# Kernel optimization log

Hardware: AMD Instinct MI355X
Metric: run time of the kernel (lower is better)

The kernel has to match this reference:

```python
import jax, jax.numpy as jnp
import numpy as np

D_MODEL = 1024
D_STATE = 16
B, L = 4, 2048


def _ln(x, g, b, eps=1e-5):
    mu = x.mean(-1, keepdims=True)
    var = ((x - mu) ** 2).mean(-1, keepdims=True)
    return (x - mu) * jax.lax.rsqrt(var + eps) * g + b


def _selective_ssm(x, dt_w, dt_b, Bp_w, Bp_b, Cp_w, Cp_b, A_log, D_p):
    # x: (B, L, D)
    delta = jax.nn.softplus(x @ dt_w + dt_b)          # (B, L, D)
    Bt = x @ Bp_w + Bp_b                               # (B, L, N)
    Ct = x @ Cp_w + Cp_b                               # (B, L, N)
    A = -jnp.exp(A_log)                                # (D, N)

    def step(h, inp):
        xt, dt, bt, ct = inp                            # (B,D),(B,D),(B,N),(B,N)
        dA = jnp.exp(dt[..., None] * A)                 # (B, D, N)
        dBx = dt[..., None] * bt[:, None, :] * xt[..., None]
        h = dA * h + dBx                                # (B, D, N)
        y = jnp.einsum('bdn,bn->bd', h, ct)
        return h, y

    xs = (jnp.swapaxes(x, 0, 1), jnp.swapaxes(delta, 0, 1),
          jnp.swapaxes(Bt, 0, 1), jnp.swapaxes(Ct, 0, 1))
    h0 = jnp.zeros((x.shape[0], D_MODEL, D_STATE), dtype=x.dtype)
    _, ys = jax.lax.scan(step, h0, xs)                  # (L, B, D)
    return jnp.swapaxes(ys, 0, 1) + D_p * x


def _forward(x, ln1_g, ln1_b, ln_g, ln_b, w1_w, w1_b, v1_w, v1_b, w2_w, w2_b,
             conv_w, dt_w, dt_b, Bp_w, Bp_b, Cp_w, Cp_b, A_log, D_p,
             ln2_g, ln2_b, ff1_w, ff1_b, ff2_w, ff2_b):
    res = x
    xn = _ln(x, ln1_g, ln1_b)
    # --- MambaLayer ---
    xm = _ln(xn, ln_g, ln_b)
    x1 = xm @ w1_w + w1_b                               # (B, L, D)
    x1t = jnp.swapaxes(x1, 1, 2)                        # (B, D, L)
    xc = jax.lax.conv_general_dilated(
        x1t, conv_w, window_strides=(1,), padding=[(1, 1)],
        feature_group_count=D_MODEL,
        dimension_numbers=('NCH', 'OIH', 'NCH'))
    xc = jax.nn.silu(jnp.swapaxes(xc, 1, 2))            # (B, L, D)
    y = _selective_ssm(xc, dt_w, dt_b, Bp_w, Bp_b, Cp_w, Cp_b, A_log, D_p)
    v = jax.nn.silu(xm @ v1_w + v1_b)
    mo = (y * v) @ w2_w + w2_b
    # --- residual + FFN ---
    x = mo + res
    res2 = x
    xn2 = _ln(x, ln2_g, ln2_b)
    h = jax.nn.gelu(xn2 @ ff1_w + ff1_b, approximate=False)
    return h @ ff2_w + ff2_b + res2


def setup_inputs() -> dict:
    key = jax.random.key(0)
    ks = jax.random.split(key, 16)
    s = 0.02
    d, n = D_MODEL, D_STATE
    inp = {
        'x': jax.random.normal(ks[0], (B, L, d), jnp.float32),
        'ln1_g': jnp.ones((d,), jnp.float32), 'ln1_b': jnp.zeros((d,), jnp.float32),
        'ln_g': jnp.ones((d,), jnp.float32), 'ln_b': jnp.zeros((d,), jnp.float32),
        'w1_w': jax.random.normal(ks[1], (d, d), jnp.float32) * s,
        'w1_b': jnp.zeros((d,), jnp.float32),
        'v1_w': jax.random.normal(ks[2], (d, d), jnp.float32) * s,
        'v1_b': jnp.zeros((d,), jnp.float32),
        'w2_w': jax.random.normal(ks[3], (d, d), jnp.float32) * s,
        'w2_b': jnp.zeros((d,), jnp.float32),
        'conv_w': jax.random.normal(ks[4], (d, 1, 3), jnp.float32) * s,
        'dt_w': jax.random.normal(ks[5], (d, d), jnp.float32) * s,
        'dt_b': jnp.zeros((d,), jnp.float32),
        'Bp_w': jax.random.normal(ks[6], (d, n), jnp.float32) * s,
        'Bp_b': jnp.zeros((n,), jnp.float32),
        'Cp_w': jax.random.normal(ks[7], (d, n), jnp.float32) * s,
        'Cp_b': jnp.zeros((n,), jnp.float32),
        'A_log': jnp.tile(jnp.log(jnp.arange(1, n + 1, dtype=jnp.float32)), (d, 1)),
        'D_p': jnp.ones((d,), jnp.float32),
        'ln2_g': jnp.ones((d,), jnp.float32), 'ln2_b': jnp.zeros((d,), jnp.float32),
        'ff1_w': jax.random.normal(ks[8], (d, 3 * d), jnp.float32) * s,
        'ff1_b': jnp.zeros((3 * d,), jnp.float32),
        'ff2_w': jax.random.normal(ks[9], (3 * d, d), jnp.float32) * s,
        'ff2_b': jnp.zeros((d,), jnp.float32),
    }
    return inp


def reference(x, ln1_g, ln1_b, ln_g, ln_b, w1_w, w1_b, v1_w, v1_b, w2_w, w2_b,
              conv_w, dt_w, dt_b, Bp_w, Bp_b, Cp_w, Cp_b, A_log, D_p,
              ln2_g, ln2_b, ff1_w, ff1_b, ff2_w, ff2_b):
    return _forward(x, ln1_g, ln1_b, ln_g, ln_b, w1_w, w1_b, v1_w, v1_b, w2_w,
                    w2_b, conv_w, dt_w, dt_b, Bp_w, Bp_b, Cp_w, Cp_b, A_log,
                    D_p, ln2_g, ln2_b, ff1_w, ff1_b, ff2_w, ff2_b)
```

## Files before the change

kernel.cpp:

```cpp
#include <hip/hip_runtime.h>

typedef unsigned short u16;
typedef __attribute__((ext_vector_type(8))) short short8;
typedef __attribute__((ext_vector_type(4))) float f32x4;
typedef __attribute__((ext_vector_type(4))) unsigned short u16x4;

#define SEQ 2048
#define DM 1024
#define NTOK 8192
#define CH 64
#define NCH 32

__device__ __forceinline__ float b2f(u16 u) {
  union { float f; unsigned int i; } x; x.i = ((unsigned int)u) << 16; return x.f;
}
__device__ __forceinline__ u16 f2b(float f) {
  union { float f; unsigned int i; } x; x.f = f;
  unsigned int i = x.i;
  unsigned int r = (i + 0x7FFFu + ((i >> 16) & 1u)) >> 16;
  return (u16)r;
}

__device__ __forceinline__ void gload16(const u16* g, u16* l) {
  __builtin_amdgcn_global_load_lds(
      (const __attribute__((address_space(1))) void*)g,
      (__attribute__((address_space(3))) void*)l, 16, 0, 0);
}

__global__ __launch_bounds__(256)
void wtrans(const float* __restrict__ in, u16* __restrict__ out,
            int K, int N, int rowOff, int ldOut)
{
  __shared__ float tile[32][33];
  const int n0 = blockIdx.x * 32;
  const int k0 = blockIdx.y * 32;
  const int tx = threadIdx.x, ty = threadIdx.y;
#pragma unroll
  for (int i = 0; i < 32; i += 8) {
    int k = k0 + ty + i, n = n0 + tx;
    tile[ty + i][tx] = (k < K && n < N) ? in[(long)k * N + n] : 0.f;
  }
  __syncthreads();
#pragma unroll
  for (int i = 0; i < 32; i += 8) {
    int n = n0 + ty + i, k = k0 + tx;
    if (n < N && k < K) out[(long)(rowOff + n) * ldOut + k] = f2b(tile[tx][ty + i]);
  }
}

__global__ __launch_bounds__(256)
void small_trans(const float* __restrict__ Bp, const float* __restrict__ Cp,
                 u16* __restrict__ wcatT)
{
  int t = blockIdx.x * 256 + threadIdx.x;
  int n = t >> 10, k = t & 1023;
  wcatT[(long)(1024 + n) * 1024 + k] = f2b(Bp[(long)k * 16 + n]);
  wcatT[(long)(1040 + n) * 1024 + k] = f2b(Cp[(long)k * 16 + n]);
}

__device__ __forceinline__ void blockReduce2(float& a, float& b, float* s)
{
#pragma unroll
  for (int off = 32; off > 0; off >>= 1) {
    a += __shfl_xor(a, off);
    b += __shfl_xor(b, off);
  }
  const int lane = threadIdx.x & 63, wid = threadIdx.x >> 6;
  __syncthreads();
  if (lane == 0) { s[wid] = a; s[4 + wid] = b; }
  __syncthreads();
  a = s[0] + s[1] + s[2] + s[3];
  b = s[4] + s[5] + s[6] + s[7];
}

__global__ __launch_bounds__(256)
void ln_ln_kernel(const float* __restrict__ x, const float* __restrict__ g1,
                  const float* __restrict__ b1, const float* __restrict__ g2,
                  const float* __restrict__ b2, u16* __restrict__ out)
{
  __shared__ float sred[8];
  const long row = blockIdx.x;
  const int t = threadIdx.x;
  const float4 xv = ((const float4*)(x + row * DM))[t];
  float s = xv.x + xv.y + xv.z + xv.w;
  float sq = xv.x * xv.x + xv.y * xv.y + xv.z * xv.z + xv.w * xv.w;
  blockReduce2(s, sq, sred);
  const float mu = s * (1.f / DM);
  const float rs = rsqrtf(sq * (1.f / DM) - mu * mu + 1e-5f);
  const float4 g1v = ((const float4*)g1)[t];
  const float4 b1v = ((const float4*)b1)[t];
  float xn[4];
  xn[0] = (xv.x - mu) * rs * g1v.x + b1v.x;
  xn[1] = (xv.y - mu) * rs * g1v.y + b1v.y;
  xn[2] = (xv.z - mu) * rs * g1v.z + b1v.z;
  xn[3] = (xv.w - mu) * rs * g1v.w + b1v.w;
  float s2 = xn[0] + xn[1] + xn[2] + xn[3];
  float sq2 = xn[0] * xn[0] + xn[1] * xn[1] + xn[2] * xn[2] + xn[3] * xn[3];
  blockReduce2(s2, sq2, sred);
  const float mu2 = s2 * (1.f / DM);
  const float rs2 = rsqrtf(sq2 * (1.f / DM) - mu2 * mu2 + 1e-5f);
  const float4 g2v = ((const float4*)g2)[t];
  const float4 b2v = ((const float4*)b2)[t];
  u16x4 o;
  o[0] = f2b((xn[0] - mu2) * rs2 * g2v.x + b2v.x);
  o[1] = f2b((xn[1] - mu2) * rs2 * g2v.y + b2v.y);
  o[2] = f2b((xn[2] - mu2) * rs2 * g2v.z + b2v.z);
  o[3] = f2b((xn[3] - mu2) * rs2 * g2v.w + b2v.w);
  *(u16x4*)(out + row * DM + t * 4) = o;
}

__global__ __launch_bounds__(256)
void ln_kernel(const float* __restrict__ x, const float* __restrict__ g,
               const float* __restrict__ b, u16* __restrict__ out)
{
  __shared__ float sred[8];
  const long row = blockIdx.x;
  const int t = threadIdx.x;
  const float4 xv = ((const float4*)(x + row * DM))[t];
  float s = xv.x + xv.y + xv.z + xv.w;
  float sq = xv.x * xv.x + xv.y * xv.y + xv.z * xv.z + xv.w * xv.w;
  blockReduce2(s, sq, sred);
  const float mu = s * (1.f / DM);
  const float rs = rsqrtf(sq * (1.f / DM) - mu * mu + 1e-5f);
  const float4 gv = ((const float4*)g)[t];
  const float4 bv = ((const float4*)b)[t];
  u16x4 o;
  o[0] = f2b((xv.x - mu) * rs * gv.x + bv.x);
  o[1] = f2b((xv.y - mu) * rs * gv.y + bv.y);
  o[2] = f2b((xv.z - mu) * rs * gv.z + bv.z);
  o[3] = f2b((xv.w - mu) * rs * gv.w + bv.w);
  *(u16x4*)(out + row * DM + t * 4) = o;
}

__global__ __launch_bounds__(256)
void conv_silu_kernel(const u16* __restrict__ x1, const float* __restrict__ w,
                      u16* __restrict__ xc)
{
  const long i8 = (long)blockIdx.x * 256 + threadIdx.x;
  const long base = i8 * 8;
  const int d0 = (int)(base & (DM - 1));
  const long m = base >> 10;
  const int l = (int)(m & (SEQ - 1));
  const short8 cv = *(const short8*)(x1 + base);
  short8 lv = {}, rv = {};
  if (l > 0) lv = *(const short8*)(x1 + base - DM);
  if (l < SEQ - 1) rv = *(const short8*)(x1 + base + DM);
  short8 o;
#pragma unroll
  for (int j = 0; j < 8; ++j) {
    const int d = d0 + j;
    const float a = b2f((u16)lv[j]) * w[d * 3 + 0] + b2f((u16)cv[j]) * w[d * 3 + 1]
                  + b2f((u16)rv[j]) * w[d * 3 + 2];
    o[j] = (short)f2b(a / (1.f + __expf(-a)));
  }
  *(short8*)(xc + base) = o;
}

template <int MODE>
__global__ __launch_bounds__(256)
void gemm_bt(const u16* __restrict__ A, const u16* __restrict__ BT,
             const float* __restrict__ bias, const float* __restrict__ bias2,
             const float* __restrict__ bias3, const float* __restrict__ resid,
             void* __restrict__ outp, void* __restrict__ outp2,
             int K, int ldOut, int nbx)
{
  __shared__ u16 lds_a[2][4096];
  __shared__ u16 lds_b[2][4096];
  const int t = threadIdx.x;
  const int lane = t & 63;
  const int wid = t >> 6;
  const int wr = wid >> 1, wc = wid & 1;

  int bid = blockIdx.x;
  const int qch = gridDim.x >> 3;
  bid = (bid & 7) * qch + (bid >> 3);
  const long brow = (long)(bid / nbx) * 128;
  const long bcol = (long)(bid % nbx) * 128;

  f32x4 acc[4][4] = {};

  const int srow = t >> 2;
  const int sslot = (t & 3) ^ ((t >> 3) & 3);
  const u16* aPtr = A + (brow + srow) * (long)K + sslot * 8;
  const u16* bPtr = BT + (bcol + srow) * (long)K + sslot * 8;
  u16* la = &lds_a[0][t * 8];
  u16* lb = &lds_b[0][t * 8];
  const long rowStep = 64L * K;
  const int nk = K >> 5;

  const int rslot = (lane >> 4) ^ ((lane >> 1) & 3);
  const int koff = rslot * 8;
  const int arow = wr * 64 + (lane & 15);
  const int brw = wc * 64 + (lane & 15);

#define STAGE(kt, buf)                                              \
  {                                                                 \
    const int k0_ = (kt) << 5;                                      \
    gload16(aPtr + k0_, la + (buf) * 4096);                         \
    gload16(aPtr + rowStep + k0_, la + (buf) * 4096 + 2048);        \
    gload16(bPtr + k0_, lb + (buf) * 4096);                         \
    gload16(bPtr + rowStep + k0_, lb + (buf) * 4096 + 2048);        \
  }

  STAGE(0, 0);
  __syncthreads();
  int cur = 0;
  for (int kt = 0; kt < nk; ++kt) {
    if (kt + 1 < nk) STAGE(kt + 1, cur ^ 1);
    short8 af[4], bfr[4];
#pragma unroll
    for (int m = 0; m < 4; ++m)
      af[m] = *(const short8*)&lds_a[cur][(arow + m * 16) * 32 + koff];
#pragma unroll
    for (int n = 0; n < 4; ++n)
      bfr[n] = *(const short8*)&lds_b[cur][(brw + n * 16) * 32 + koff];
#pragma unroll
    for (int m = 0; m < 4; ++m)
#pragma unroll
      for (int n = 0; n < 4; ++n)
        acc[m][n] = __builtin_amdgcn_mfma_f32_16x16x32_bf16(af[m], bfr[n], acc[m][n], 0, 0, 0);
    __syncthreads();
    cur ^= 1;
  }
#undef STAGE

  const int cc = lane & 15;
  const int r0 = (lane >> 4) * 4;
#pragma unroll
  for (int m = 0; m < 4; ++m) {
#pragma unroll
    for (int n = 0; n < 4; ++n) {
      const long col = bcol + wc * 64 + n * 16 + cc;
#pragma unroll
      for (int r = 0; r < 4; ++r) {
        const long row = brow + wr * 64 + m * 16 + r0 + r;
        float val = acc[m][n][r];
        if constexpr (MODE == 4) {
          if (col < 1024) {
            val += bias[col];
            val = (val > 20.f) ? val : log1pf(__expf(val));
            ((float*)outp)[row * 1152 + col] = val;
          } else if (col < 1040) {
            ((float*)outp)[row * 1152 + col] = val + bias2[col - 1024];
          } else if (col < 1056) {
            ((float*)outp)[row * 1152 + col] = val + bias3[col - 1040];
          }
        } else if constexpr (MODE == 5) {
          if (col < 1024) {
            val += bias[col];
            ((u16*)outp)[row * 1024 + col] = f2b(val);
          } else {
            val += bias2[col - 1024];
            val = val / (1.f + __expf(-val));
            ((u16*)outp2)[row * 1024 + col - 1024] = f2b(val);
          }
        } else {
          val += bias[col];
          if constexpr (MODE == 2) val = 0.5f * val * (1.f + erff(val * 0.70710678118f));
          if constexpr (MODE == 3) {
            ((float*)outp)[row * ldOut + col] = val + resid[row * ldOut + col];
          } else {
            ((u16*)outp)[row * ldOut + col] = f2b(val);
          }
        }
      }
    }
  }
}

__global__ __launch_bounds__(256)
void scan_pass1(const u16* __restrict__ xc, const float* __restrict__ dtbc,
                const float* __restrict__ A_log, float* __restrict__ hloc,
                float* __restrict__ sdt)
{
  const int bx = blockIdx.x;
  const int b = bx >> 9;
  const int ch = (bx >> 4) & 31;
  const int dBase = (bx & 15) * 64;
  const int t = threadIdx.x;
  const int dl = t >> 2;
  const int q = t & 3;
  const int d = dBase + dl;

  __shared__ float s_b[32][16];
  __shared__ float s_dt[32][64];
  __shared__ u16 s_x[32][64];

  float Areg[4];
#pragma unroll
  for (int j = 0; j < 4; ++j) Areg[j] = -__expf(A_log[d * 16 + q * 4 + j]);
  float h[4] = {0.f, 0.f, 0.f, 0.f};
  float sAcc = 0.f;
  const long mBase = (long)b * SEQ + ch * CH;

  for (int c0 = 0; c0 < CH; c0 += 32) {
#pragma unroll
    for (int i = 0; i < 2; ++i) {
      int idx = i * 256 + t;
      int s = idx >> 4, j = idx & 15;
      s_b[s][j] = dtbc[(mBase + c0 + s) * 1152 + 1024 + j];
    }
#pragma unroll
    for (int i = 0; i < 8; ++i) {
      int idx = i * 256 + t;
      int s = idx >> 6, j = idx & 63;
      long m = mBase + c0 + s;
      s_dt[s][j] = dtbc[m * 1152 + dBase + j];
      s_x[s][j] = xc[m * DM + dBase + j];
    }
    __syncthreads();
#pragma unroll 4
    for (int s = 0; s < 32; ++s) {
      const float dt = s_dt[s][dl];
      const float p = dt * b2f(s_x[s][dl]);
      sAcc += dt;
#pragma unroll
      for (int j = 0; j < 4; ++j)
        h[j] = __expf(dt * Areg[j]) * h[j] + p * s_b[s][q * 4 + j];
    }
    __syncthreads();
  }
  const long base = (((long)b * NCH + ch) * 1024 + d) * 16 + q * 4;
  float4 hv; hv.x = h[0]; hv.y = h[1]; hv.z = h[2]; hv.w = h[3];
  *(float4*)&hloc[base] = hv;
  if (q == 0) sdt[((long)b * NCH + ch) * 1024 + d] = sAcc;
}

__global__ __launch_bounds__(256)
void scan_pass2(const float* __restrict__ A_log, const float* __restrict__ sdt,
                const float* __restrict__ hloc, float* __restrict__ hin)
{
  const int tid = blockIdx.x * 256 + threadIdx.x;
  const int b = tid >> 14;
  const int dn = tid & 16383;
  const int d = dn >> 4;
  const float A = -__expf(A_log[dn]);
  float h = 0.f;
  for (int c = 0; c < NCH; ++c) {
    const long idx = (((long)b * NCH + c) << 14) + dn;
    hin[idx] = h;
    h = __expf(A * sdt[((long)b * NCH + c) * 1024 + d]) * h + hloc[idx];
  }
}

__global__ __launch_bounds__(256)
void scan_pass3(const u16* __restrict__ xc, const float* __restrict__ dtbc,
                const u16* __restrict__ vg, const float* __restrict__ A_log,
                const float* __restrict__ D_p, const float* __restrict__ hin,
                u16* __restrict__ yv)
{
  const int bx = blockIdx.x;
  const int b = bx >> 9;
  const int ch = (bx >> 4) & 31;
  const int dBase = (bx & 15) * 64;
  const int t = threadIdx.x;
  const int dl = t >> 2;
  const int q = t & 3;
  const int d = dBase + dl;

  __shared__ float s_bc[32][32];
  __shared__ float s_dt[32][64];
  __shared__ u16 s_x[32][64];
  __shared__ u16 s_v[32][64];
  __shared__ u16 s_y[32][64];

  float Areg[4];
#pragma unroll
  for (int j = 0; j < 4; ++j) Areg[j] = -__expf(A_log[d * 16 + q * 4 + j]);
  const float Dp = D_p[d];
  const float4 hv = *(const float4*)&hin[(((long)b * NCH + ch) * 1024 + d) * 16 + q * 4];
  float h[4] = {hv.x, hv.y, hv.z, hv.w};

  const long mBase = (long)b * SEQ + ch * CH;

  for (int c0 = 0; c0 < CH; c0 += 32) {
#pragma unroll
    for (int i = 0; i < 4; ++i) {
      int idx = i * 256 + t;
      int s = idx >> 5, j = idx & 31;
      s_bc[s][j] = dtbc[(mBase + c0 + s) * 1152 + 1024 + j];
    }
#pragma unroll
    for (int i = 0; i < 8; ++i) {
      int idx = i * 256 + t;
      int s = idx >> 6, j = idx & 63;
      long m = mBase + c0 + s;
      s_dt[s][j] = dtbc[m * 1152 + dBase + j];
      s_x[s][j] = xc[m * DM + dBase + j];
      s_v[s][j] = vg[m * DM + dBase + j];
    }
    __syncthreads();
#pragma unroll 4
    for (int s = 0; s < 32; ++s) {
      const float dt = s_dt[s][dl];
      const float xt = b2f(s_x[s][dl]);
      const float p = dt * xt;
      float y = 0.f;
#pragma unroll
      for (int j = 0; j < 4; ++j) {
        const float dA = __expf(dt * Areg[j]);
        h[j] = dA * h[j] + p * s_bc[s][q * 4 + j];
        y = fmaf(h[j], s_bc[s][16 + q * 4 + j], y);
      }
      y += __shfl_xor(y, 1);
      y += __shfl_xor(y, 2);
      if (q == 0) s_y[s][dl] = f2b((y + Dp * xt) * b2f(s_v[s][dl]));
    }
    __syncthreads();
#pragma unroll
    for (int i = 0; i < 8; ++i) {
      int idx = i * 256 + t;
      int s = idx >> 6, j = idx & 63;
      yv[(mBase + c0 + s) * DM + dBase + j] = s_y[s][j];
    }
    __syncthreads();
  }
}

extern "C" void kernel_launch(void* const* d_in, const int* in_sizes, int n_in,
                              void* d_out, int out_size, void* d_ws, size_t ws_size,
                              hipStream_t stream)
{
  (void)in_sizes; (void)n_in; (void)out_size; (void)ws_size;
  const float* x      = (const float*)d_in[0];
  const float* ln1_g  = (const float*)d_in[1];
  const float* ln1_b  = (const float*)d_in[2];
  const float* ln_g   = (const float*)d_in[3];
  const float* ln_b   = (const float*)d_in[4];
  const float* w1_w   = (const float*)d_in[5];
  const float* w1_b   = (const float*)d_in[6];
  const float* v1_w   = (const float*)d_in[7];
  const float* v1_b   = (const float*)d_in[8];
  const float* w2_w   = (const float*)d_in[9];
  const float* w2_b   = (const float*)d_in[10];
  const float* conv_w = (const float*)d_in[11];
  const float* dt_w   = (const float*)d_in[12];
  const float* dt_b   = (const float*)d_in[13];
  const float* Bp_w   = (const float*)d_in[14];
  const float* Bp_b   = (const float*)d_in[15];
  const float* Cp_w   = (const float*)d_in[16];
  const float* Cp_b   = (const float*)d_in[17];
  const float* A_log  = (const float*)d_in[18];
  const float* D_p    = (const float*)d_in[19];
  const float* ln2_g  = (const float*)d_in[20];
  const float* ln2_b  = (const float*)d_in[21];
  const float* ff1_w  = (const float*)d_in[22];
  const float* ff1_b  = (const float*)d_in[23];
  const float* ff2_w  = (const float*)d_in[24];
  const float* ff2_b  = (const float*)d_in[25];

  char* ws = (char*)d_ws;
  size_t cur = 0;
  auto alloc = [&](size_t bytes) -> void* {
    void* p = ws + cur;
    cur = (cur + bytes + 255) & ~(size_t)255;
    return p;
  };

  u16* wv1T  = (u16*)alloc((size_t)2048 * 1024 * 2);
  u16* w2T   = (u16*)alloc((size_t)1024 * 1024 * 2);
  u16* wcatT = (u16*)alloc((size_t)1152 * 1024 * 2);
  u16* ff1T  = (u16*)alloc((size_t)3072 * 1024 * 2);
  u16* ff2T  = (u16*)alloc((size_t)1024 * 3072 * 2);
  u16* xm    = (u16*)alloc((size_t)NTOK * DM * 2);
  u16* x1b   = (u16*)alloc((size_t)NTOK * DM * 2);
  u16* vb    = (u16*)alloc((size_t)NTOK * DM * 2);
  u16* xcb   = (u16*)alloc((size_t)NTOK * DM * 2);
  float* dtbc = (float*)alloc((size_t)NTOK * 1152 * 4);
  float* x2  = (float*)alloc((size_t)NTOK * DM * 4);
  float* hloc = (float*)alloc((size_t)4 * NCH * 1024 * 16 * 4);
  float* hin  = (float*)alloc((size_t)4 * NCH * 1024 * 16 * 4);
  float* sdtb = (float*)alloc((size_t)4 * NCH * 1024 * 4);
  u16* yvb  = xm;
  u16* xn2  = x1b;
  u16* hb   = xcb;

  const dim3 tb32(32, 8);
  wtrans<<<dim3(32, 32), tb32, 0, stream>>>(w1_w, wv1T, 1024, 1024, 0, 1024);
  wtrans<<<dim3(32, 32), tb32, 0, stream>>>(v1_w, wv1T, 1024, 1024, 1024, 1024);
  wtrans<<<dim3(32, 32), tb32, 0, stream>>>(w2_w, w2T, 1024, 1024, 0, 1024);
  wtrans<<<dim3(32, 32), tb32, 0, stream>>>(dt_w, wcatT, 1024, 1024, 0, 1024);
  small_trans<<<64, 256, 0, stream>>>(Bp_w, Cp_w, wcatT);
  hipMemsetAsync(wcatT + (size_t)1056 * 1024, 0, (size_t)96 * 1024 * 2, stream);
  wtrans<<<dim3(96, 32), tb32, 0, stream>>>(ff1_w, ff1T, 1024, 3072, 0, 1024);
  wtrans<<<dim3(32, 96), tb32, 0, stream>>>(ff2_w, ff2T, 3072, 1024, 0, 3072);

  ln_ln_kernel<<<NTOK, 256, 0, stream>>>(x, ln1_g, ln1_b, ln_g, ln_b, xm);

  gemm_bt<5><<<1024, 256, 0, stream>>>(xm, wv1T, w1_b, v1_b, nullptr, nullptr,
                                       x1b, vb, 1024, 1024, 16);

  conv_silu_kernel<<<(NTOK * DM) / (256 * 8), 256, 0, stream>>>(x1b, conv_w, xcb);

  gemm_bt<4><<<576, 256, 0, stream>>>(xcb, wcatT, dt_b, Bp_b, Cp_b, nullptr,
                                      dtbc, nullptr, 1024, 1152, 9);

  scan_pass1<<<2048, 256, 0, stream>>>(xcb, dtbc, A_log, hloc, sdtb);
  scan_pass2<<<256, 256, 0, stream>>>(A_log, sdtb, hloc, hin);
  scan_pass3<<<2048, 256, 0, stream>>>(xcb, dtbc, vb, A_log, D_p, hin, yvb);

  gemm_bt<3><<<512, 256, 0, stream>>>(yvb, w2T, w2_b, nullptr, nullptr, x,
                                      x2, nullptr, 1024, 1024, 8);

  ln_kernel<<<NTOK, 256, 0, stream>>>(x2, ln2_g, ln2_b, xn2);

  gemm_bt<2><<<1536, 256, 0, stream>>>(xn2, ff1T, ff1_b, nullptr, nullptr, nullptr,
                                       hb, nullptr, 1024, 3072, 24);

  gemm_bt<3><<<512, 256, 0, stream>>>(hb, ff2T, ff2_b, nullptr, nullptr, x2,
                                      d_out, nullptr, 3072, 1024, 8);
}
```

Baseline: 470.8 us.

## Enlarge GEMM tile to 256x128 with 512 threads and 4-stage LDS pipeline

The bf16 GEMM now runs 512-thread blocks (8 waves) covering 256x128 output tiles, so each B tile is shared across twice as many rows. The double-buffered LDS scheme is replaced by a 4-buffer ring that prefetches three k-steps ahead, using explicit vmcnt waits and raw barriers in place of __syncthreads. This aims to hide global-load latency and cut B-operand traffic. In exchange, grid sizes are halved, which lowers the number of blocks per CU, and LDS use rises to 96 KB per block, which limits occupancy.

```diff
diff --git a/kernel.cpp b/kernel.cpp
--- a/kernel.cpp
+++ b/kernel.cpp
@@ -157,15 +157,15 @@
 }
 
 template <int MODE>
-__global__ __launch_bounds__(256)
+__global__ __launch_bounds__(512)
 void gemm_bt(const u16* __restrict__ A, const u16* __restrict__ BT,
              const float* __restrict__ bias, const float* __restrict__ bias2,
              const float* __restrict__ bias3, const float* __restrict__ resid,
              void* __restrict__ outp, void* __restrict__ outp2,
              int K, int ldOut, int nbx)
 {
-  __shared__ u16 lds_a[2][4096];
-  __shared__ u16 lds_b[2][4096];
+  __shared__ u16 lds_a[4][8192];
+  __shared__ u16 lds_b[4][4096];
   const int t = threadIdx.x;
   const int lane = t & 63;
   const int wid = t >> 6;
@@ -174,7 +174,7 @@
   int bid = blockIdx.x;
   const int qch = gridDim.x >> 3;
   bid = (bid & 7) * qch + (bid >> 3);
-  const long brow = (long)(bid / nbx) * 128;
+  const long brow = (long)(bid / nbx) * 256;
   const long bcol = (long)(bid % nbx) * 128;
 
   f32x4 acc[4][4] = {};
@@ -183,9 +183,7 @@
   const int sslot = (t & 3) ^ ((t >> 3) & 3);
   const u16* aPtr = A + (brow + srow) * (long)K + sslot * 8;
   const u16* bPtr = BT + (bcol + srow) * (long)K + sslot * 8;
-  u16* la = &lds_a[0][t * 8];
-  u16* lb = &lds_b[0][t * 8];
-  const long rowStep = 64L * K;
+  const long rowStep = 128L * K;
   const int nk = K >> 5;
 
   const int rslot = (lane >> 4) ^ ((lane >> 1) & 3);
@@ -196,31 +194,42 @@
 #define STAGE(kt, buf)                                              \
   {                                                                 \
     const int k0_ = (kt) << 5;                                      \
-    gload16(aPtr + k0_, la + (buf) * 4096);                         \
-    gload16(aPtr + rowStep + k0_, la + (buf) * 4096 + 2048);        \
-    gload16(bPtr + k0_, lb + (buf) * 4096);                         \
-    gload16(bPtr + rowStep + k0_, lb + (buf) * 4096 + 2048);        \
+    gload16(aPtr + k0_, &lds_a[buf][t * 8]);                        \
+    gload16(aPtr + rowStep + k0_, &lds_a[buf][4096 + t * 8]);       \
+    gload16(bPtr + k0_, &lds_b[buf][t * 8]);                        \
   }
 
   STAGE(0, 0);
-  __syncthreads();
-  int cur = 0;
+  STAGE(1, 1);
+  STAGE(2, 2);
+  asm volatile("s_waitcnt vmcnt(6)" ::: "memory");
+  __builtin_amdgcn_s_barrier();
+  asm volatile("" ::: "memory");
+
   for (int kt = 0; kt < nk; ++kt) {
-    if (kt + 1 < nk) STAGE(kt + 1, cur ^ 1);
+    const int buf = kt & 3;
+    if (kt + 3 < nk) STAGE(kt + 3, (kt + 3) & 3);
     short8 af[4], bfr[4];
 #pragma unroll
     for (int m = 0; m < 4; ++m)
-      af[m] = *(const short8*)&lds_a[cur][(arow + m * 16) * 32 + koff];
+      af[m] = *(const short8*)&lds_a[buf][(arow + m * 16) * 32 + koff];
 #pragma unroll
     for (int n = 0; n < 4; ++n)
-      bfr[n] = *(const short8*)&lds_b[cur][(brw + n * 16) * 32 + koff];
+      bfr[n] = *(const short8*)&lds_b[buf][(brw + n * 16) * 32 + koff];
 #pragma unroll
     for (int m = 0; m < 4; ++m)
 #pragma unroll
       for (int n = 0; n < 4; ++n)
         acc[m][n] = __builtin_amdgcn_mfma_f32_16x16x32_bf16(af[m], bfr[n], acc[m][n], 0, 0, 0);
-    __syncthreads();
-    cur ^= 1;
+    if (kt + 1 < nk) {
+      const int staged = (kt + 3 < nk) ? kt + 3 : nk - 1;
+      const int beyond = staged - (kt + 1);
+      if (beyond == 2)      asm volatile("s_waitcnt vmcnt(6)" ::: "memory");
+      else if (beyond == 1) asm volatile("s_waitcnt vmcnt(3)" ::: "memory");
+      else                  asm volatile("s_waitcnt vmcnt(0)" ::: "memory");
+      __builtin_amdgcn_s_barrier();
+      asm volatile("" ::: "memory");
+    }
   }
 #undef STAGE
 
@@ -487,26 +496,26 @@
 
   ln_ln_kernel<<<NTOK, 256, 0, stream>>>(x, ln1_g, ln1_b, ln_g, ln_b, xm);
 
-  gemm_bt<5><<<1024, 256, 0, stream>>>(xm, wv1T, w1_b, v1_b, nullptr, nullptr,
-                                       x1b, vb, 1024, 1024, 16);
+  gemm_bt<5><<<512, 512, 0, stream>>>(xm, wv1T, w1_b, v1_b, nullptr, nullptr,
+                                      x1b, vb, 1024, 1024, 16);
 
   conv_silu_kernel<<<(NTOK * DM) / (256 * 8), 256, 0, stream>>>(x1b, conv_w, xcb);
 
-  gemm_bt<4><<<576, 256, 0, stream>>>(xcb, wcatT, dt_b, Bp_b, Cp_b, nullptr,
+  gemm_bt<4><<<288, 512, 0, stream>>>(xcb, wcatT, dt_b, Bp_b, Cp_b, nullptr,
                                       dtbc, nullptr, 1024, 1152, 9);
 
   scan_pass1<<<2048, 256, 0, stream>>>(xcb, dtbc, A_log, hloc, sdtb);
   scan_pass2<<<256, 256, 0, stream>>>(A_log, sdtb, hloc, hin);
   scan_pass3<<<2048, 256, 0, stream>>>(xcb, dtbc, vb, A_log, D_p, hin, yvb);
 
-  gemm_bt<3><<<512, 256, 0, stream>>>(yvb, w2T, w2_b, nullptr, nullptr, x,
+  gemm_bt<3><<<256, 512, 0, stream>>>(yvb, w2T, w2_b, nullptr, nullptr, x,
                                       x2, nullptr, 1024, 1024, 8);
 
   ln_kernel<<<NTOK, 256, 0, stream>>>(x2, ln2_g, ln2_b, xn2);
 
-  gemm_bt<2><<<1536, 256, 0, stream>>>(xn2, ff1T, ff1_b, nullptr, nullptr, nullptr,
-                                       hb, nullptr, 1024, 3072, 24);
-
-  gemm_bt<3><<<512, 256, 0, stream>>>(hb, ff2T, ff2_b, nullptr, nullptr, x2,
+  gemm_bt<2><<<768, 512, 0, stream>>>(xn2, ff1T, ff1_b, nullptr, nullptr, nullptr,
+                                      hb, nullptr, 1024, 3072, 24);
+
+  gemm_bt<3><<<256, 512, 0, stream>>>(hb, ff2T, ff2_b, nullptr, nullptr, x2,
                                       d_out, nullptr, 3072, 1024, 8);
 }
```

Result: slower. 573.7 us (+21.8%).

## Add 256x256-tile 8-wave GEMM with ping-pong LDS pipeline for w1/v1 and ff1

Applied to the files above, without the earlier changes.

Introduces gemm8p, a 512-thread kernel computing 256x256 output tiles from double-buffered, XOR-swizzled LDS halves. Global-to-LDS loads for the next k-tile are interleaved with MFMA phases, and s_setprio raises priority during the math sections. It replaces the 128x128-tile gemm_bt for the fused w1/v1 projection and the GELU ff1 GEMM, with the block index remapped across 8 groups. The aim is more operand reuse per byte loaded and better overlap of loads with compute, at the cost of fewer, larger blocks, more registers, and heavy LDS use.

```diff
diff --git a/kernel.cpp b/kernel.cpp
--- a/kernel.cpp
+++ b/kernel.cpp
@@ -245,7 +245,166 @@
           } else if (col < 1056) {
             ((float*)outp)[row * 1152 + col] = val + bias3[col - 1040];
           }
-        } else if constexpr (MODE == 5) {
+        } else {
+          val += bias[col];
+          if constexpr (MODE == 3) {
+            ((float*)outp)[row * ldOut + col] = val + resid[row * ldOut + col];
+          } else {
+            ((u16*)outp)[row * ldOut + col] = f2b(val);
+          }
+        }
+      }
+    }
+  }
+}
+
+template <int MODE>
+__global__ __launch_bounds__(512, 2)
+void gemm8p(const u16* __restrict__ A, const u16* __restrict__ BT,
+            const float* __restrict__ bias, const float* __restrict__ bias2,
+            void* __restrict__ outp, void* __restrict__ outp2,
+            int K, int ldOut, int nbx)
+{
+  __shared__ u16 LA[2][2][8192];
+  __shared__ u16 LB[2][2][8192];
+  const int t = threadIdx.x;
+  const int lane = t & 63;
+  const int wid = t >> 6;
+  const int wr = wid >> 2;
+  const int wc = wid & 3;
+
+  int bid = blockIdx.x;
+  const int qch = gridDim.x >> 3;
+  bid = (bid & 7) * qch + (bid >> 3);
+  const long brow = (long)(bid / nbx) * 256;
+  const long bcol = (long)(bid % nbx) * 256;
+
+  f32x4 acc[8][4] = {};
+
+  const int srow = t >> 3;
+  const int sc = (t & 7) ^ (srow & 7);
+  const u16* aBase = A + (brow + srow) * (long)K + sc * 8;
+  const u16* bBase = BT + (bcol + srow) * (long)K + sc * 8;
+  const long halfStep = 128L * (long)K;
+  const long rowStep = 64L * (long)K;
+  const int nt = K >> 6;
+
+  const int l15 = lane & 15, l4 = lane >> 4, l7 = lane & 7;
+  const int aoff0 = (wr * 64 + l15) * 128 + ((l4 ^ l7) * 16);
+  const int aoff1 = (wr * 64 + l15) * 128 + (((4 | l4) ^ l7) * 16);
+  const int boff0 = (wc * 32 + l15) * 128 + ((l4 ^ l7) * 16);
+  const int boff1 = (wc * 32 + l15) * 128 + (((4 | l4) ^ l7) * 16);
+
+#define SGA(kt_, h_) { const int p_ = (kt_) & 1;                                    \
+    gload16(aBase + (h_) * halfStep + (long)(kt_) * 64, &LA[p_][h_][t * 8]);        \
+    gload16(aBase + (h_) * halfStep + rowStep + (long)(kt_) * 64,                   \
+            &LA[p_][h_][4096 + t * 8]); }
+#define SGB(kt_, h_) { const int p_ = (kt_) & 1;                                    \
+    gload16(bBase + (h_) * halfStep + (long)(kt_) * 64, &LB[p_][h_][t * 8]);        \
+    gload16(bBase + (h_) * halfStep + rowStep + (long)(kt_) * 64,                   \
+            &LB[p_][h_][4096 + t * 8]); }
+
+  SGA(0, 0); SGB(0, 1); SGA(0, 1); SGB(0, 0); SGA(1, 0); SGB(1, 1);
+  asm volatile("s_waitcnt vmcnt(4)" ::: "memory");
+  __builtin_amdgcn_s_barrier();
+
+  short8 af[8], bl[4], bh[4];
+  for (int kt = 0; kt < nt; ++kt) {
+    const int par = kt & 1;
+    const char* bAlo = (const char*)&LA[par][0][0];
+    const char* bAhi = (const char*)&LA[par][1][0];
+    const char* bBlo = (const char*)&LB[par][0][0];
+    const char* bBhi = (const char*)&LB[par][1][0];
+
+#pragma unroll
+    for (int m2 = 0; m2 < 4; ++m2) {
+      af[m2 * 2 + 0] = *(const short8*)(bAlo + aoff0 + m2 * 2048);
+      af[m2 * 2 + 1] = *(const short8*)(bAlo + aoff1 + m2 * 2048);
+    }
+#pragma unroll
+    for (int n2 = 0; n2 < 2; ++n2) {
+      bl[n2 * 2 + 0] = *(const short8*)(bBlo + boff0 + n2 * 2048);
+      bl[n2 * 2 + 1] = *(const short8*)(bBlo + boff1 + n2 * 2048);
+    }
+    if (kt + 1 < nt) SGA(kt + 1, 1);
+    __builtin_amdgcn_s_barrier();
+    __builtin_amdgcn_s_setprio(1);
+#pragma unroll
+    for (int m2 = 0; m2 < 4; ++m2)
+#pragma unroll
+      for (int n2 = 0; n2 < 2; ++n2) {
+        acc[m2][n2] = __builtin_amdgcn_mfma_f32_16x16x32_bf16(af[m2*2+0], bl[n2*2+0], acc[m2][n2], 0, 0, 0);
+        acc[m2][n2] = __builtin_amdgcn_mfma_f32_16x16x32_bf16(af[m2*2+1], bl[n2*2+1], acc[m2][n2], 0, 0, 0);
+      }
+    __builtin_amdgcn_s_setprio(0);
+    __builtin_amdgcn_s_barrier();
+
+#pragma unroll
+    for (int n2 = 0; n2 < 2; ++n2) {
+      bh[n2 * 2 + 0] = *(const short8*)(bBhi + boff0 + n2 * 2048);
+      bh[n2 * 2 + 1] = *(const short8*)(bBhi + boff1 + n2 * 2048);
+    }
+    if (kt + 1 < nt) SGB(kt + 1, 0);
+    __builtin_amdgcn_s_barrier();
+    __builtin_amdgcn_s_setprio(1);
+#pragma unroll
+    for (int m2 = 0; m2 < 4; ++m2)
+#pragma unroll
+      for (int n2 = 0; n2 < 2; ++n2) {
+        acc[m2][2 + n2] = __builtin_amdgcn_mfma_f32_16x16x32_bf16(af[m2*2+0], bh[n2*2+0], acc[m2][2 + n2], 0, 0, 0);
+        acc[m2][2 + n2] = __builtin_amdgcn_mfma_f32_16x16x32_bf16(af[m2*2+1], bh[n2*2+1], acc[m2][2 + n2], 0, 0, 0);
+      }
+    __builtin_amdgcn_s_setprio(0);
+    __builtin_amdgcn_s_barrier();
+
+#pragma unroll
+    for (int m2 = 0; m2 < 4; ++m2) {
+      af[m2 * 2 + 0] = *(const short8*)(bAhi + aoff0 + m2 * 2048);
+      af[m2 * 2 + 1] = *(const short8*)(bAhi + aoff1 + m2 * 2048);
+    }
+    if (kt + 2 < nt) SGA(kt + 2, 0);
+    __builtin_amdgcn_s_barrier();
+    __builtin_amdgcn_s_setprio(1);
+#pragma unroll
+    for (int m2 = 0; m2 < 4; ++m2)
+#pragma unroll
+      for (int n2 = 0; n2 < 2; ++n2) {
+        acc[4 + m2][2 + n2] = __builtin_amdgcn_mfma_f32_16x16x32_bf16(af[m2*2+0], bh[n2*2+0], acc[4 + m2][2 + n2], 0, 0, 0);
+        acc[4 + m2][2 + n2] = __builtin_amdgcn_mfma_f32_16x16x32_bf16(af[m2*2+1], bh[n2*2+1], acc[4 + m2][2 + n2], 0, 0, 0);
+      }
+    __builtin_amdgcn_s_setprio(0);
+    __builtin_amdgcn_s_barrier();
+
+    if (kt + 2 < nt) SGB(kt + 2, 1);
+    __builtin_amdgcn_s_setprio(1);
+#pragma unroll
+    for (int m2 = 0; m2 < 4; ++m2)
+#pragma unroll
+      for (int n2 = 0; n2 < 2; ++n2) {
+        acc[4 + m2][n2] = __builtin_amdgcn_mfma_f32_16x16x32_bf16(af[m2*2+0], bl[n2*2+0], acc[4 + m2][n2], 0, 0, 0);
+        acc[4 + m2][n2] = __builtin_amdgcn_mfma_f32_16x16x32_bf16(af[m2*2+1], bl[n2*2+1], acc[4 + m2][n2], 0, 0, 0);
+      }
+    __builtin_amdgcn_s_setprio(0);
+    if (kt + 2 < nt)      asm volatile("s_waitcnt vmcnt(4)" ::: "memory");
+    else if (kt + 1 < nt) asm volatile("s_waitcnt vmcnt(0)" ::: "memory");
+    if (kt + 1 < nt) __builtin_amdgcn_s_barrier();
+  }
+#undef SGA
+#undef SGB
+
+  const int cc = lane & 15;
+  const int r0 = (lane >> 4) * 4;
+#pragma unroll
+  for (int m = 0; m < 8; ++m) {
+    const long row0 = brow + (m >> 2) * 128 + wr * 64 + (m & 3) * 16 + r0;
+#pragma unroll
+    for (int n = 0; n < 4; ++n) {
+      const long col = bcol + (n >> 1) * 128 + wc * 32 + (n & 1) * 16 + cc;
+#pragma unroll
+      for (int r = 0; r < 4; ++r) {
+        const long row = row0 + r;
+        float val = acc[m][n][r];
+        if constexpr (MODE == 5) {
           if (col < 1024) {
             val += bias[col];
             ((u16*)outp)[row * 1024 + col] = f2b(val);
@@ -256,12 +415,8 @@
           }
         } else {
           val += bias[col];
-          if constexpr (MODE == 2) val = 0.5f * val * (1.f + erff(val * 0.70710678118f));
-          if constexpr (MODE == 3) {
-            ((float*)outp)[row * ldOut + col] = val + resid[row * ldOut + col];
-          } else {
-            ((u16*)outp)[row * ldOut + col] = f2b(val);
-          }
+          val = 0.5f * val * (1.f + erff(val * 0.70710678118f));
+          ((u16*)outp)[row * ldOut + col] = f2b(val);
         }
       }
     }
@@ -487,8 +642,7 @@
 
   ln_ln_kernel<<<NTOK, 256, 0, stream>>>(x, ln1_g, ln1_b, ln_g, ln_b, xm);
 
-  gemm_bt<5><<<1024, 256, 0, stream>>>(xm, wv1T, w1_b, v1_b, nullptr, nullptr,
-                                       x1b, vb, 1024, 1024, 16);
+  gemm8p<5><<<256, 512, 0, stream>>>(xm, wv1T, w1_b, v1_b, x1b, vb, 1024, 1024, 8);
 
   conv_silu_kernel<<<(NTOK * DM) / (256 * 8), 256, 0, stream>>>(x1b, conv_w, xcb);
 
@@ -504,8 +658,8 @@
 
   ln_kernel<<<NTOK, 256, 0, stream>>>(x2, ln2_g, ln2_b, xn2);
 
-  gemm_bt<2><<<1536, 256, 0, stream>>>(xn2, ff1T, ff1_b, nullptr, nullptr, nullptr,
-                                       hb, nullptr, 1024, 3072, 24);
+  gemm8p<2><<<384, 512, 0, stream>>>(xn2, ff1T, ff1_b, nullptr, hb, nullptr,
+                                     1024, 3072, 12);
 
   gemm_bt<3><<<512, 256, 0, stream>>>(hb, ff2T, ff2_b, nullptr, nullptr, x2,
                                       d_out, nullptr, 3072, 1024, 8);
```

New measurement: 475.4 us. No clear change (+1.0%).

## Compute local scan outputs in pass1 and replace pass3 recurrence with correction

Applied to the files above, without the earlier changes.

The first scan pass now also emits the chunk-local output y (with the D skip term) and the cumulative delta per position, both stored as bf16. The third pass no longer reruns the recurrence; it adds a closed-form correction C·exp(A·cumdelta)·h_in and applies the gate. This removes the serial recurrence from pass3 at the cost of extra bf16 writes and reads, and bf16 rounding of the cumulative delta may cost precision. Separately, exact erff in the GELU epilogue is replaced with a polynomial approximation, and the weight-transpose launches and the memset are merged into fewer kernels.

```diff
diff --git a/kernel.cpp b/kernel.cpp
--- a/kernel.cpp
+++ b/kernel.cpp
@@ -27,6 +27,16 @@
       (__attribute__((address_space(3))) void*)l, 16, 0, 0);
 }
 
+__device__ __forceinline__ float gelu_f(float v) {
+  const float z = fabsf(v) * 0.70710678118f;
+  const float t = __builtin_amdgcn_rcpf(1.f + 0.3275911f * z);
+  float poly = ((((1.061405429f * t - 1.453152027f) * t + 1.421413741f) * t
+                 - 0.284496736f) * t + 0.254829592f) * t;
+  float e = 1.f - poly * __expf(-z * z);
+  float erfv = (v < 0.f) ? -e : e;
+  return 0.5f * v * (1.f + erfv);
+}
+
 __global__ __launch_bounds__(256)
 void wtrans(const float* __restrict__ in, u16* __restrict__ out,
             int K, int N, int rowOff, int ldOut)
@@ -49,6 +59,32 @@
 }
 
 __global__ __launch_bounds__(256)
+void wtrans4(const float* __restrict__ s0, const float* __restrict__ s1,
+             const float* __restrict__ s2, const float* __restrict__ s3,
+             u16* __restrict__ d0, u16* __restrict__ d1,
+             u16* __restrict__ d2, u16* __restrict__ d3)
+{
+  __shared__ float tile[32][33];
+  const float* in; u16* out;
+  switch (blockIdx.z) {
+    case 0: in = s0; out = d0; break;
+    case 1: in = s1; out = d1; break;
+    case 2: in = s2; out = d2; break;
+    default: in = s3; out = d3; break;
+  }
+  const int n0 = blockIdx.x * 32;
+  const int k0 = blockIdx.y * 32;
+  const int tx = threadIdx.x, ty = threadIdx.y;
+#pragma unroll
+  for (int i = 0; i < 32; i += 8)
+    tile[ty + i][tx] = in[(long)(k0 + ty + i) * 1024 + n0 + tx];
+  __syncthreads();
+#pragma unroll
+  for (int i = 0; i < 32; i += 8)
+    out[(long)(n0 + ty + i) * 1024 + k0 + tx] = f2b(tile[tx][ty + i]);
+}
+
+__global__ __launch_bounds__(256)
 void small_trans(const float* __restrict__ Bp, const float* __restrict__ Cp,
                  u16* __restrict__ wcatT)
 {
@@ -56,6 +92,9 @@
   int n = t >> 10, k = t & 1023;
   wcatT[(long)(1024 + n) * 1024 + k] = f2b(Bp[(long)k * 16 + n]);
   wcatT[(long)(1040 + n) * 1024 + k] = f2b(Cp[(long)k * 16 + n]);
+#pragma unroll
+  for (int i = 0; i < 6; ++i)
+    wcatT[(long)1056 * 1024 + i * 16384 + t] = 0;
 }
 
 __device__ __forceinline__ void blockReduce2(float& a, float& b, float* s)
@@ -256,7 +295,7 @@
           }
         } else {
           val += bias[col];
-          if constexpr (MODE == 2) val = 0.5f * val * (1.f + erff(val * 0.70710678118f));
+          if constexpr (MODE == 2) val = gelu_f(val);
           if constexpr (MODE == 3) {
             ((float*)outp)[row * ldOut + col] = val + resid[row * ldOut + col];
           } else {
@@ -270,8 +309,9 @@
 
 __global__ __launch_bounds__(256)
 void scan_pass1(const u16* __restrict__ xc, const float* __restrict__ dtbc,
-                const float* __restrict__ A_log, float* __restrict__ hloc,
-                float* __restrict__ sdt)
+                const float* __restrict__ A_log, const float* __restrict__ D_p,
+                float* __restrict__ hloc, float* __restrict__ sdt,
+                u16* __restrict__ ylb, u16* __restrict__ cdb)
 {
   const int bx = blockIdx.x;
   const int b = bx >> 9;
@@ -282,23 +322,26 @@
   const int q = t & 3;
   const int d = dBase + dl;
 
-  __shared__ float s_b[32][16];
+  __shared__ float s_bc[32][32];
   __shared__ float s_dt[32][64];
   __shared__ u16 s_x[32][64];
+  __shared__ u16 s_yl[32][64];
+  __shared__ u16 s_cd[32][64];
 
   float Areg[4];
 #pragma unroll
   for (int j = 0; j < 4; ++j) Areg[j] = -__expf(A_log[d * 16 + q * 4 + j]);
+  const float Dp = D_p[d];
   float h[4] = {0.f, 0.f, 0.f, 0.f};
   float sAcc = 0.f;
   const long mBase = (long)b * SEQ + ch * CH;
 
   for (int c0 = 0; c0 < CH; c0 += 32) {
 #pragma unroll
-    for (int i = 0; i < 2; ++i) {
+    for (int i = 0; i < 4; ++i) {
       int idx = i * 256 + t;
-      int s = idx >> 4, j = idx & 15;
-      s_b[s][j] = dtbc[(mBase + c0 + s) * 1152 + 1024 + j];
+      int s = idx >> 5, j = idx & 31;
+      s_bc[s][j] = dtbc[(mBase + c0 + s) * 1152 + 1024 + j];
     }
 #pragma unroll
     for (int i = 0; i < 8; ++i) {
@@ -312,11 +355,28 @@
 #pragma unroll 4
     for (int s = 0; s < 32; ++s) {
       const float dt = s_dt[s][dl];
-      const float p = dt * b2f(s_x[s][dl]);
+      const float xt = b2f(s_x[s][dl]);
+      const float p = dt * xt;
       sAcc += dt;
-#pragma unroll
-      for (int j = 0; j < 4; ++j)
-        h[j] = __expf(dt * Areg[j]) * h[j] + p * s_b[s][q * 4 + j];
+      float y = 0.f;
+#pragma unroll
+      for (int j = 0; j < 4; ++j) {
+        h[j] = __expf(dt * Areg[j]) * h[j] + p * s_bc[s][q * 4 + j];
+        y = fmaf(h[j], s_bc[s][16 + q * 4 + j], y);
+      }
+      y += __shfl_xor(y, 1);
+      y += __shfl_xor(y, 2);
+      if (q == 0) s_yl[s][dl] = f2b(y + Dp * xt);
+      if (q == 1) s_cd[s][dl] = f2b(sAcc);
+    }
+    __syncthreads();
+#pragma unroll
+    for (int i = 0; i < 8; ++i) {
+      int idx = i * 256 + t;
+      int s = idx >> 6, j = idx & 63;
+      long m = mBase + c0 + s;
+      ylb[m * DM + dBase + j] = s_yl[s][j];
+      cdb[m * DM + dBase + j] = s_cd[s][j];
     }
     __syncthreads();
   }
@@ -344,10 +404,10 @@
 }
 
 __global__ __launch_bounds__(256)
-void scan_pass3(const u16* __restrict__ xc, const float* __restrict__ dtbc,
-                const u16* __restrict__ vg, const float* __restrict__ A_log,
-                const float* __restrict__ D_p, const float* __restrict__ hin,
-                u16* __restrict__ yv)
+void scan_fix(const float* __restrict__ dtbc, const u16* __restrict__ ylb,
+              const u16* __restrict__ cdb, const u16* __restrict__ vg,
+              const float* __restrict__ A_log, const float* __restrict__ hin,
+              u16* __restrict__ yv)
 {
   const int bx = blockIdx.x;
   const int b = bx >> 9;
@@ -358,60 +418,55 @@
   const int q = t & 3;
   const int d = dBase + dl;
 
-  __shared__ float s_bc[32][32];
-  __shared__ float s_dt[32][64];
-  __shared__ u16 s_x[32][64];
+  __shared__ float s_c[32][16];
+  __shared__ u16 s_cd[32][64];
+  __shared__ u16 s_yl[32][64];
   __shared__ u16 s_v[32][64];
-  __shared__ u16 s_y[32][64];
+  __shared__ u16 s_o[32][64];
 
   float Areg[4];
 #pragma unroll
   for (int j = 0; j < 4; ++j) Areg[j] = -__expf(A_log[d * 16 + q * 4 + j]);
-  const float Dp = D_p[d];
-  const float4 hv = *(const float4*)&hin[(((long)b * NCH + ch) * 1024 + d) * 16 + q * 4];
-  float h[4] = {hv.x, hv.y, hv.z, hv.w};
+  const float4 hv4 = *(const float4*)&hin[(((long)b * NCH + ch) * 1024 + d) * 16 + q * 4];
+  const float hv[4] = {hv4.x, hv4.y, hv4.z, hv4.w};
 
   const long mBase = (long)b * SEQ + ch * CH;
 
   for (int c0 = 0; c0 < CH; c0 += 32) {
 #pragma unroll
-    for (int i = 0; i < 4; ++i) {
+    for (int i = 0; i < 2; ++i) {
       int idx = i * 256 + t;
-      int s = idx >> 5, j = idx & 31;
-      s_bc[s][j] = dtbc[(mBase + c0 + s) * 1152 + 1024 + j];
+      int s = idx >> 4, j = idx & 15;
+      s_c[s][j] = dtbc[(mBase + c0 + s) * 1152 + 1040 + j];
     }
 #pragma unroll
     for (int i = 0; i < 8; ++i) {
       int idx = i * 256 + t;
       int s = idx >> 6, j = idx & 63;
       long m = mBase + c0 + s;
-      s_dt[s][j] = dtbc[m * 1152 + dBase + j];
-      s_x[s][j] = xc[m * DM + dBase + j];
+      s_cd[s][j] = cdb[m * DM + dBase + j];
+      s_yl[s][j] = ylb[m * DM + dBase + j];
       s_v[s][j] = vg[m * DM + dBase + j];
     }
     __syncthreads();
 #pragma unroll 4
     for (int s = 0; s < 32; ++s) {
-      const float dt = s_dt[s][dl];
-      const float xt = b2f(s_x[s][dl]);
-      const float p = dt * xt;
-      float y = 0.f;
-#pragma unroll
-      for (int j = 0; j < 4; ++j) {
-        const float dA = __expf(dt * Areg[j]);
-        h[j] = dA * h[j] + p * s_bc[s][q * 4 + j];
-        y = fmaf(h[j], s_bc[s][16 + q * 4 + j], y);
-      }
-      y += __shfl_xor(y, 1);
-      y += __shfl_xor(y, 2);
-      if (q == 0) s_y[s][dl] = f2b((y + Dp * xt) * b2f(s_v[s][dl]));
+      const float cd = b2f(s_cd[s][dl]);
+      float corr = 0.f;
+#pragma unroll
+      for (int j = 0; j < 4; ++j)
+        corr = fmaf(s_c[s][q * 4 + j] * hv[j], __expf(Areg[j] * cd), corr);
+      corr += __shfl_xor(corr, 1);
+      corr += __shfl_xor(corr, 2);
+      if (q == 0)
+        s_o[s][dl] = f2b((b2f(s_yl[s][dl]) + corr) * b2f(s_v[s][dl]));
     }
     __syncthreads();
 #pragma unroll
     for (int i = 0; i < 8; ++i) {
       int idx = i * 256 + t;
       int s = idx >> 6, j = idx & 63;
-      yv[(mBase + c0 + s) * DM + dBase + j] = s_y[s][j];
+      yv[(mBase + c0 + s) * DM + dBase + j] = s_o[s][j];
     }
     __syncthreads();
   }
@@ -473,15 +528,15 @@
   float* sdtb = (float*)alloc((size_t)4 * NCH * 1024 * 4);
   u16* yvb  = xm;
   u16* xn2  = x1b;
+  u16* ylb  = x1b;
+  u16* cdb  = (u16*)x2;
   u16* hb   = xcb;
 
   const dim3 tb32(32, 8);
-  wtrans<<<dim3(32, 32), tb32, 0, stream>>>(w1_w, wv1T, 1024, 1024, 0, 1024);
-  wtrans<<<dim3(32, 32), tb32, 0, stream>>>(v1_w, wv1T, 1024, 1024, 1024, 1024);
-  wtrans<<<dim3(32, 32), tb32, 0, stream>>>(w2_w, w2T, 1024, 1024, 0, 1024);
-  wtrans<<<dim3(32, 32), tb32, 0, stream>>>(dt_w, wcatT, 1024, 1024, 0, 1024);
+  wtrans4<<<dim3(32, 32, 4), tb32, 0, stream>>>(w1_w, v1_w, w2_w, dt_w,
+                                                wv1T, wv1T + (size_t)1024 * 1024,
+                                                w2T, wcatT);
   small_trans<<<64, 256, 0, stream>>>(Bp_w, Cp_w, wcatT);
-  hipMemsetAsync(wcatT + (size_t)1056 * 1024, 0, (size_t)96 * 1024 * 2, stream);
   wtrans<<<dim3(96, 32), tb32, 0, stream>>>(ff1_w, ff1T, 1024, 3072, 0, 1024);
   wtrans<<<dim3(32, 96), tb32, 0, stream>>>(ff2_w, ff2T, 3072, 1024, 0, 3072);
 
@@ -495,9 +550,9 @@
   gemm_bt<4><<<576, 256, 0, stream>>>(xcb, wcatT, dt_b, Bp_b, Cp_b, nullptr,
                                       dtbc, nullptr, 1024, 1152, 9);
 
-  scan_pass1<<<2048, 256, 0, stream>>>(xcb, dtbc, A_log, hloc, sdtb);
+  scan_pass1<<<2048, 256, 0, stream>>>(xcb, dtbc, A_log, D_p, hloc, sdtb, ylb, cdb);
   scan_pass2<<<256, 256, 0, stream>>>(A_log, sdtb, hloc, hin);
-  scan_pass3<<<2048, 256, 0, stream>>>(xcb, dtbc, vb, A_log, D_p, hin, yvb);
+  scan_fix<<<2048, 256, 0, stream>>>(dtbc, ylb, cdb, vb, A_log, hin, yvb);
 
   gemm_bt<3><<<512, 256, 0, stream>>>(yvb, w2T, w2_b, nullptr, nullptr, x,
                                       x2, nullptr, 1024, 1024, 8);
```

After: 460.5 us. 1.02x faster.
